# Performance work log

Hardware: AMD Instinct MI355X
Metric: run time of the kernel (lower is better)

The kernel has to match this reference:

```python
import jax, jax.numpy as jnp
import numpy as np

NUM_HEADS = 16
HEAD_DIM = 64
HIDDEN = NUM_HEADS * HEAD_DIM  # 1024
BATCH, SEQ = 4, 2048


def setup_inputs() -> dict:
    key = jax.random.key(0)
    k1, k2, k3, k4 = jax.random.split(key, 4)
    hidden_states = jax.random.normal(k1, (BATCH, SEQ, HIDDEN), dtype=jnp.float32)
    attention_mask = jnp.arange(SEQ)[None, :] < int(SEQ * 0.9)
    attention_mask = jnp.broadcast_to(attention_mask, (BATCH, SEQ))
    s_in = 1.0 / np.sqrt(HIDDEN)
    Wqkv = jax.random.normal(k2, (HIDDEN, 3 * HIDDEN), dtype=jnp.float32) * s_in
    Wout = jax.random.normal(k3, (HIDDEN, HIDDEN), dtype=jnp.float32) * s_in
    bout = jnp.zeros((HIDDEN,), dtype=jnp.float32)
    return {"hidden_states": hidden_states, "attention_mask": attention_mask,
            "Wqkv": Wqkv, "Wout": Wout, "bout": bout}


def reference(hidden_states, attention_mask, Wqkv, Wout, bout):
    B, S, H = hidden_states.shape
    qkv = hidden_states @ Wqkv  # [B,S,3*H]
    qkv = qkv.reshape(B, S, 3, NUM_HEADS, HEAD_DIM)
    qkv = jnp.transpose(qkv, (2, 0, 3, 1, 4))  # [3,B,nh,S,hd]
    q, k, v = qkv[0], qkv[1], qkv[2]
    scale = 1.0 / jnp.sqrt(jnp.float32(HEAD_DIM))
    attn = jnp.einsum('bhid,bhjd->bhij', q, k) * scale  # [B,nh,S,S]
    bias = jnp.where(attention_mask[:, None, None, :], 0.0,
                     jnp.finfo(jnp.float32).min)
    attn = attn + bias
    attn = jax.nn.softmax(attn, axis=-1)
    out = jnp.einsum('bhij,bhjd->bhid', attn, v)  # [B,nh,S,hd]
    out = jnp.transpose(out, (0, 2, 1, 3)).reshape(B, S, H)
    return out @ Wout + bout
```

## Files before the change

kernel.cpp:

```cpp
#include <hip/hip_runtime.h>


typedef short bh8 __attribute__((ext_vector_type(8)));
typedef short bh4 __attribute__((ext_vector_type(4)));
typedef float f32x4 __attribute__((ext_vector_type(4)));

#define B_ 4
#define S_ 2048
#define NH_ 16
#define HD_ 64
#define H_ 1024

__device__ float g_biasf[B_ * S_];
__device__ int g_tl[B_ * 33];

__device__ inline short f2bf(float f) {
    unsigned u = __builtin_bit_cast(unsigned, f);
    u = (u + 0x7fffu + ((u >> 16) & 1u)) >> 16;
    return (short)u;
}

__device__ inline unsigned pk2bf(float a, float b) {
#if __has_builtin(__builtin_amdgcn_cvt_pk_bf16_f32)
    auto r = __builtin_amdgcn_cvt_pk_bf16_f32(a, b);
    return __builtin_bit_cast(unsigned, r);
#else
    unsigned ua = __builtin_bit_cast(unsigned, a) + 0x8000u;
    unsigned ub = __builtin_bit_cast(unsigned, b) + 0x8000u;
    return __builtin_amdgcn_perm(ub, ua, 0x07060302);
#endif
}

__global__ void prep_all(const float* __restrict__ hidden, const float* __restrict__ Wqkv,
                         const float* __restrict__ Wout, const int* __restrict__ mask,
                         short* __restrict__ Xbf, short* __restrict__ WqkvT,
                         short* __restrict__ WoutT, float qs) {
    __shared__ float tile[32][33];
    int bi = blockIdx.x, tid = threadIdx.x;

    if (bi < 8192) {
        int i = (bi * 256 + tid) * 4;
        float4 v = *(const float4*)(hidden + i);
        union { short s[4]; unsigned long long u; } r;
        r.s[0] = f2bf(v.x); r.s[1] = f2bf(v.y); r.s[2] = f2bf(v.z); r.s[3] = f2bf(v.w);
        *(unsigned long long*)(Xbf + i) = r.u;
        return;
    }
    if (bi < 12288) {
        const float* in; short* out; int N, qcols, idx;
        if (bi < 11264) { in = Wqkv; out = WqkvT; N = 3 * H_; qcols = H_; idx = bi - 8192;
        } else          { in = Wout; out = WoutT; N = H_;    qcols = 0;  idx = bi - 11264; }
        int xt = (bi < 11264) ? 96 : 32;
        int n0 = (idx % xt) * 32, k0 = (idx / xt) * 32;
        int tx = tid & 31, ty = tid >> 5;
#pragma unroll
        for (int i = 0; i < 32; i += 8)
            tile[ty + i][tx] = in[(long)(k0 + ty + i) * N + n0 + tx];
        __syncthreads();
#pragma unroll
        for (int i = 0; i < 32; i += 8) {
            int n = n0 + ty + i;
            float v = tile[tx][ty + i];
            if (n < qcols) v *= qs;
            out[(long)n * H_ + k0 + tx] = f2bf(v);
        }
        return;
    }
    if (bi < 12320) {
        int i = (bi - 12288) * 256 + tid;
        g_biasf[i] = mask[i] ? 0.0f : -1e30f;
        return;
    }
    {
        int b = bi - 12320;
        if (tid < 64) {
            int t = tid, flag = 0;
            if (t < 32) {
                bool anyA = false, anyM = false;
                for (int i = 0; i < 64; ++i) {
                    int m = mask[b * S_ + t * 64 + i];
                    anyA |= (m != 0); anyM |= (m == 0);
                }
                flag = anyA ? (anyM ? 1 : 2) : 0;
            }
            unsigned long long act = __ballot(flag != 0);
            int pos = __popcll(act & ((1ull << t) - 1ull));
            if (flag) g_tl[b * 33 + 1 + pos] = t | (flag << 16);
            if (t == 0) g_tl[b * 33] = __popcll(act);
        }
    }
}

__global__ __launch_bounds__(256, 2) void gemm_bf16(
    const short* __restrict__ A, const short* __restrict__ Bt,
    int M, int N, int K, int mode,
    short* __restrict__ qk, short* __restrict__ vt,
    const float* __restrict__ bias, float* __restrict__ out) {
    __shared__ short smem[128 * 136];
    short* sA[2] = { smem, smem + 4096 };
    short* sB[2] = { smem + 8192, smem + 12288 };
    int tid = threadIdx.x;
    int lane = tid & 63, wid = tid >> 6;
    int quad = lane >> 4, l15 = lane & 15;
    int wy = wid >> 1, wx = wid & 1;
    int m0 = blockIdx.y * 128, n0 = blockIdx.x * 128;

    f32x4 acc[4][4] = {};
    const short* Ag = A + (long)m0 * K;
    const short* Bg = Bt + (long)n0 * K;

    for (int k0 = 0; k0 < K; k0 += 64) {
#pragma unroll
        for (int half = 0; half < 2; ++half) {
#pragma unroll
            for (int i = 0; i < 2; ++i) {
                int flat = i * 256 + tid;
                int r = flat >> 2, c = (flat & 3) << 3;
                __builtin_amdgcn_global_load_lds(
                    (const __attribute__((address_space(1))) void*)(Ag + (long)r * K + k0 + half * 32 + c),
                    (__attribute__((address_space(3))) void*)(sA[half] + i * 2048 + wid * 512),
                    16, 0, 0);
                __builtin_amdgcn_global_load_lds(
                    (const __attribute__((address_space(1))) void*)(Bg + (long)r * K + k0 + half * 32 + c),
                    (__attribute__((address_space(3))) void*)(sB[half] + i * 2048 + wid * 512),
                    16, 0, 0);
            }
        }
        __syncthreads();
#pragma unroll
        for (int half = 0; half < 2; ++half) {
            bh8 af[4], bfr[4];
#pragma unroll
            for (int mi = 0; mi < 4; ++mi)
                af[mi] = *(const bh8*)(sA[half] + (wy * 64 + mi * 16 + l15) * 32 + quad * 8);
#pragma unroll
            for (int ni = 0; ni < 4; ++ni)
                bfr[ni] = *(const bh8*)(sB[half] + (wx * 64 + ni * 16 + l15) * 32 + quad * 8);
#pragma unroll
            for (int mi = 0; mi < 4; ++mi)
#pragma unroll
                for (int ni = 0; ni < 4; ++ni)
                    acc[mi][ni] = __builtin_amdgcn_mfma_f32_16x16x32_bf16(af[mi], bfr[ni], acc[mi][ni], 0, 0, 0);
        }
        __syncthreads();
    }

    if (mode == 0) {
        bool isV = (n0 >= 2048);
#pragma unroll
        for (int mi = 0; mi < 4; ++mi)
#pragma unroll
            for (int ni = 0; ni < 4; ++ni) {
                int c = wx * 64 + ni * 16 + l15;
                int rb = wy * 64 + mi * 16 + quad * 4;
                if (isV) {
                    unsigned lo = pk2bf(acc[mi][ni][0], acc[mi][ni][1]);
                    unsigned hi = pk2bf(acc[mi][ni][2], acc[mi][ni][3]);
                    uint2 uu = {lo, hi};
                    *(bh4*)(smem + c * 136 + rb) = __builtin_bit_cast(bh4, uu);
                } else {
#pragma unroll
                    for (int reg = 0; reg < 4; ++reg)
                        smem[(rb + reg) * 136 + c] = f2bf(acc[mi][ni][reg]);
                }
            }
        __syncthreads();
        int b = m0 >> 11, sbase = m0 & 2047;
#pragma unroll
        for (int j = 0; j < 8; ++j) {
            int f = (j * 256 + tid) * 8;
            int i0 = f >> 7, i1 = f & 127;
            bh8 v = *(const bh8*)(smem + i0 * 136 + i1);
            if (isV) {
                int cc = n0 - 2048 + i0;
                int h = cc >> 6, d = cc & 63;
                *(bh8*)(vt + ((long)(b * NH_ + h) * HD_ + d) * S_ + sbase + i1) = v;
            } else {
                *(bh8*)(qk + (long)(m0 + i0) * 2048 + n0 + i1) = v;
            }
        }
    } else {
#pragma unroll
        for (int mi = 0; mi < 4; ++mi)
#pragma unroll
            for (int ni = 0; ni < 4; ++ni) {
                int gc = n0 + wx * 64 + ni * 16 + l15;
                float bv = bias[gc];
#pragma unroll
                for (int reg = 0; reg < 4; ++reg) {
                    int gr = m0 + wy * 64 + mi * 16 + quad * 4 + reg;
                    out[(long)gr * N + gc] = acc[mi][ni][reg] + bv;
                }
            }
    }
}

__global__ __launch_bounds__(256, 2) void attn_fwd(
    const short* __restrict__ QK, const short* __restrict__ Vtw,
    short* __restrict__ Aout) {
    __shared__ short lK[2][64 * 72];
    __shared__ short lV[2][64 * 72];
    int tid = threadIdx.x;
    int lane = tid & 63, w = tid >> 6;
    int quad = lane >> 4, l15 = lane & 15;
    int p = blockIdx.x;
    int b = p >> 4, h = p & 15;
    int qbase = blockIdx.y * 256 + w * 64;

    const short* Kb = QK + (long)b * S_ * 2048 + 1024 + h * HD_;
    const short* Vb = Vtw + (long)p * HD_ * S_;

    int r0 = tid >> 3, g = tid & 7, c = g << 3;
    int voff = (g >> 2) * 32 + (g & 1) * 16 + ((g >> 1) & 1) * 4;
    const short* Kp0 = Kb + (long)r0 * 2048 + c;
    const short* Kp1 = Kp0 + 32l * 2048;
    const short* Vp0 = Vb + (long)r0 * S_ + c;
    const short* Vp1 = Vp0 + 32l * S_;

    bh8 qf[4][2];
#pragma unroll
    for (int mi = 0; mi < 4; ++mi)
#pragma unroll
        for (int ks = 0; ks < 2; ++ks)
            qf[mi][ks] = *(const bh8*)(QK + (long)(b * S_ + qbase + mi * 16 + l15) * 2048
                                       + h * HD_ + ks * 32 + quad * 8);

    f32x4 o[4][4] = {};
    f32x4 ls[4] = {};
    const bh8 ones = {0x3F80, 0x3F80, 0x3F80, 0x3F80, 0x3F80, 0x3F80, 0x3F80, 0x3F80};

    int cnt = g_tl[b * 33];
    int e0 = g_tl[b * 33 + 1];
    int j0 = (e0 & 0xffff) << 6, flag = e0 >> 16;
    bh8 kp[2], vp[2];
    kp[0] = *(const bh8*)(Kp0 + (long)j0 * 2048);
    kp[1] = *(const bh8*)(Kp1 + (long)j0 * 2048);
    vp[0] = *(const bh8*)(Vp0 + j0);
    vp[1] = *(const bh8*)(Vp1 + j0);
    {
        *(bh8*)(lK[0] + r0 * 72 + c) = kp[0];
        *(bh8*)(lK[0] + (r0 + 32) * 72 + c) = kp[1];
        *(bh4*)(lV[0] + r0 * 72 + voff)            = __builtin_shufflevector(vp[0], vp[0], 0, 1, 2, 3);
        *(bh4*)(lV[0] + r0 * 72 + voff + 8)        = __builtin_shufflevector(vp[0], vp[0], 4, 5, 6, 7);
        *(bh4*)(lV[0] + (r0 + 32) * 72 + voff)     = __builtin_shufflevector(vp[1], vp[1], 0, 1, 2, 3);
        *(bh4*)(lV[0] + (r0 + 32) * 72 + voff + 8) = __builtin_shufflevector(vp[1], vp[1], 4, 5, 6, 7);
    }
    int cur = 0;

    for (int it = 0; it < cnt; ++it) {
        __syncthreads();
        bool more = (it + 1 < cnt);
        int nj0 = 0, nflag = 0;
        if (more) {
            int en = g_tl[b * 33 + 2 + it];
            nj0 = (en & 0xffff) << 6; nflag = en >> 16;
            kp[0] = *(const bh8*)(Kp0 + (long)nj0 * 2048);
            kp[1] = *(const bh8*)(Kp1 + (long)nj0 * 2048);
            vp[0] = *(const bh8*)(Vp0 + nj0);
            vp[1] = *(const bh8*)(Vp1 + nj0);
        }
        const short* ck = lK[cur];
        const short* cv = lV[cur];

        bh4 pf[4][4];
#pragma unroll
        for (int nj = 0; nj < 4; ++nj) {
            f32x4 scn[4] = {};
#pragma unroll
            for (int ks = 0; ks < 2; ++ks) {
                bh8 kf = *(const bh8*)(ck + (nj * 16 + l15) * 72 + ks * 32 + quad * 8);
#pragma unroll
                for (int mi = 0; mi < 4; ++mi)
                    scn[mi] = __builtin_amdgcn_mfma_f32_16x16x32_bf16(kf, qf[mi][ks], scn[mi], 0, 0, 0);
            }
            if (flag == 1) {
                f32x4 bb = *(const f32x4*)(g_biasf + b * S_ + j0 + nj * 16 + quad * 4);
#pragma unroll
                for (int mi = 0; mi < 4; ++mi) {
#pragma unroll
                    for (int r = 0; r < 4; ++r) scn[mi][r] += bb[r];
                }
            }
#pragma unroll
            for (int mi = 0; mi < 4; ++mi) {
                unsigned u0 = pk2bf(__builtin_amdgcn_exp2f(scn[mi][0]),
                                    __builtin_amdgcn_exp2f(scn[mi][1]));
                unsigned u1 = pk2bf(__builtin_amdgcn_exp2f(scn[mi][2]),
                                    __builtin_amdgcn_exp2f(scn[mi][3]));
                uint2 uu = {u0, u1};
                pf[nj][mi] = __builtin_bit_cast(bh4, uu);
            }
        }

#pragma unroll
        for (int pr = 0; pr < 2; ++pr) {
            int njA = 2 * pr, njB = 2 * pr + 1;
            bh8 a[4];
#pragma unroll
            for (int mi = 0; mi < 4; ++mi)
                a[mi] = __builtin_shufflevector(pf[njA][mi], pf[njB][mi], 0, 1, 2, 3, 4, 5, 6, 7);
            __builtin_amdgcn_s_setprio(1);
#pragma unroll
            for (int mi = 0; mi < 4; ++mi)
                ls[mi] = __builtin_amdgcn_mfma_f32_16x16x32_bf16(a[mi], ones, ls[mi], 0, 0, 0);
#pragma unroll
            for (int nd = 0; nd < 4; ++nd) {
                bh8 vf = *(const bh8*)(cv + (nd * 16 + l15) * 72 + pr * 32 + quad * 8);
#pragma unroll
                for (int mi = 0; mi < 4; ++mi)
                    o[mi][nd] = __builtin_amdgcn_mfma_f32_16x16x32_bf16(a[mi], vf, o[mi][nd], 0, 0, 0);
            }
            __builtin_amdgcn_s_setprio(0);
        }

        if (more) {
            short* lk = lK[cur ^ 1];
            short* lv = lV[cur ^ 1];
            *(bh8*)(lk + r0 * 72 + c) = kp[0];
            *(bh8*)(lk + (r0 + 32) * 72 + c) = kp[1];
            *(bh4*)(lv + r0 * 72 + voff)            = __builtin_shufflevector(vp[0], vp[0], 0, 1, 2, 3);
            *(bh4*)(lv + r0 * 72 + voff + 8)        = __builtin_shufflevector(vp[0], vp[0], 4, 5, 6, 7);
            *(bh4*)(lv + (r0 + 32) * 72 + voff)     = __builtin_shufflevector(vp[1], vp[1], 0, 1, 2, 3);
            *(bh4*)(lv + (r0 + 32) * 72 + voff + 8) = __builtin_shufflevector(vp[1], vp[1], 4, 5, 6, 7);
        }
        j0 = nj0; flag = nflag; cur ^= 1;
    }

#pragma unroll
    for (int mi = 0; mi < 4; ++mi)
#pragma unroll
        for (int reg = 0; reg < 4; ++reg) {
            float inv = __builtin_amdgcn_rcpf(ls[mi][reg]);
            int s = qbase + mi * 16 + quad * 4 + reg;
#pragma unroll
            for (int nd = 0; nd < 4; ++nd) {
                int col = h * HD_ + nd * 16 + l15;
                Aout[((long)b * S_ + s) * H_ + col] = f2bf(o[mi][nd][reg] * inv);
            }
        }
}

extern "C" void kernel_launch(void* const* d_in, const int* in_sizes, int n_in,
                              void* d_out, int out_size, void* d_ws, size_t ws_size,
                              hipStream_t stream) {
    const float* hidden = (const float*)d_in[0];
    const int* mask = (const int*)d_in[1];
    const float* Wqkv = (const float*)d_in[2];
    const float* Wout = (const float*)d_in[3];
    const float* bout = (const float*)d_in[4];
    float* out = (float*)d_out;

    char* ws = (char*)d_ws;
    const size_t XBF = 0;
    const size_t WQKVT = 16777216;
    const size_t WOUTT = WQKVT + 6291456;
    const size_t QKO = WOUTT + 2097152;
    const size_t VT = QKO + 33554432;

    short* Xbf = (short*)(ws + XBF);
    short* WqkvT = (short*)(ws + WQKVT);
    short* WoutT = (short*)(ws + WOUTT);
    short* QK = (short*)(ws + QKO);
    short* Vt = (short*)(ws + VT);
    short* Aout = Xbf;

    const float Cs = 0.18033688011112042f;

    prep_all<<<dim3(12324), dim3(256), 0, stream>>>(
        hidden, Wqkv, Wout, mask, Xbf, WqkvT, WoutT, Cs);

    gemm_bf16<<<dim3(24, 64), dim3(256), 0, stream>>>(
        Xbf, WqkvT, B_ * S_, 3 * H_, H_, 0, QK, Vt, nullptr, nullptr);

    attn_fwd<<<dim3(64, 8), dim3(256), 0, stream>>>(QK, Vt, Aout);

    gemm_bf16<<<dim3(8, 64), dim3(256), 0, stream>>>(
        Aout, WoutT, B_ * S_, H_, H_, 1, nullptr, nullptr, bout, out);
}
```

Baseline: 250.5 us.

## Double-buffer GEMM LDS tiles to overlap global loads with MFMA compute

Restructures the bf16 GEMM main loop into a two-stage pipeline. The next K-tile is prefetched into the alternate LDS buffer via global_load_lds while the current tile is consumed, with explicit vmcnt waits and raw barriers replacing __syncthreads. This targets global-load latency that was previously exposed each iteration. In exchange it doubles LDS use to 64KB per block, which may limit the occupancy the launch bounds request.

```diff
diff --git a/kernel.cpp b/kernel.cpp
--- a/kernel.cpp
+++ b/kernel.cpp
@@ -91,14 +91,32 @@
     }
 }
 
+__device__ inline void gemm_stage(const short* Ag, const short* Bg, int K, int k0,
+                                  short* sAB, int tid, int wid) {
+#pragma unroll
+    for (int half = 0; half < 2; ++half) {
+#pragma unroll
+        for (int i = 0; i < 2; ++i) {
+            int flat = i * 256 + tid;
+            int r = flat >> 2, c = (flat & 3) << 3;
+            __builtin_amdgcn_global_load_lds(
+                (const __attribute__((address_space(1))) void*)(Ag + (long)r * K + k0 + half * 32 + c),
+                (__attribute__((address_space(3))) void*)(sAB + half * 4096 + i * 2048 + wid * 512),
+                16, 0, 0);
+            __builtin_amdgcn_global_load_lds(
+                (const __attribute__((address_space(1))) void*)(Bg + (long)r * K + k0 + half * 32 + c),
+                (__attribute__((address_space(3))) void*)(sAB + 8192 + half * 4096 + i * 2048 + wid * 512),
+                16, 0, 0);
+        }
+    }
+}
+
 __global__ __launch_bounds__(256, 2) void gemm_bf16(
     const short* __restrict__ A, const short* __restrict__ Bt,
     int M, int N, int K, int mode,
     short* __restrict__ qk, short* __restrict__ vt,
     const float* __restrict__ bias, float* __restrict__ out) {
-    __shared__ short smem[128 * 136];
-    short* sA[2] = { smem, smem + 4096 };
-    short* sB[2] = { smem + 8192, smem + 12288 };
+    __shared__ short smem[32768];
     int tid = threadIdx.x;
     int lane = tid & 63, wid = tid >> 6;
     int quad = lane >> 4, l15 = lane & 15;
@@ -108,41 +126,36 @@
     f32x4 acc[4][4] = {};
     const short* Ag = A + (long)m0 * K;
     const short* Bg = Bt + (long)n0 * K;
-
-    for (int k0 = 0; k0 < K; k0 += 64) {
-#pragma unroll
-        for (int half = 0; half < 2; ++half) {
-#pragma unroll
-            for (int i = 0; i < 2; ++i) {
-                int flat = i * 256 + tid;
-                int r = flat >> 2, c = (flat & 3) << 3;
-                __builtin_amdgcn_global_load_lds(
-                    (const __attribute__((address_space(1))) void*)(Ag + (long)r * K + k0 + half * 32 + c),
-                    (__attribute__((address_space(3))) void*)(sA[half] + i * 2048 + wid * 512),
-                    16, 0, 0);
-                __builtin_amdgcn_global_load_lds(
-                    (const __attribute__((address_space(1))) void*)(Bg + (long)r * K + k0 + half * 32 + c),
-                    (__attribute__((address_space(3))) void*)(sB[half] + i * 2048 + wid * 512),
-                    16, 0, 0);
-            }
-        }
-        __syncthreads();
+    int NT = K >> 6;
+
+    gemm_stage(Ag, Bg, K, 0, smem, tid, wid);
+    for (int t = 0; t < NT; ++t) {
+        int curOff = (t & 1) << 14;
+        if (t + 1 < NT) {
+            gemm_stage(Ag, Bg, K, (t + 1) << 6, smem + (curOff ^ 16384), tid, wid);
+            asm volatile("s_waitcnt vmcnt(8)" ::: "memory");
+        } else {
+            asm volatile("s_waitcnt vmcnt(0)" ::: "memory");
+        }
+        __builtin_amdgcn_s_barrier();
+        const short* sA = smem + curOff;
+        const short* sB = smem + curOff + 8192;
 #pragma unroll
         for (int half = 0; half < 2; ++half) {
             bh8 af[4], bfr[4];
 #pragma unroll
             for (int mi = 0; mi < 4; ++mi)
-                af[mi] = *(const bh8*)(sA[half] + (wy * 64 + mi * 16 + l15) * 32 + quad * 8);
+                af[mi] = *(const bh8*)(sA + half * 4096 + (wy * 64 + mi * 16 + l15) * 32 + quad * 8);
 #pragma unroll
             for (int ni = 0; ni < 4; ++ni)
-                bfr[ni] = *(const bh8*)(sB[half] + (wx * 64 + ni * 16 + l15) * 32 + quad * 8);
+                bfr[ni] = *(const bh8*)(sB + half * 4096 + (wx * 64 + ni * 16 + l15) * 32 + quad * 8);
 #pragma unroll
             for (int mi = 0; mi < 4; ++mi)
 #pragma unroll
                 for (int ni = 0; ni < 4; ++ni)
                     acc[mi][ni] = __builtin_amdgcn_mfma_f32_16x16x32_bf16(af[mi], bfr[ni], acc[mi][ni], 0, 0, 0);
         }
-        __syncthreads();
+        __builtin_amdgcn_s_barrier();
     }
 
     if (mode == 0) {
```

New measurement: 253.4 us. No clear change (+1.2%).

## Specialize QKV GEMM with 256x256 tiles, direct-to-LDS loads and block swizzle

Applied to the files above, without the earlier changes.

Splits the generic GEMM into a dedicated QKV projection kernel and an output-projection kernel. The QKV kernel uses 512 threads, 256x256 tiles, double-buffered global_load_lds staging prefetched two K-steps ahead, a swizzled block order for L2 reuse, and raised wave priority around the MFMA bursts. The goal is more data reuse per tile and load latency hidden behind the MFMAs. The costs are 128KB of LDS per block, which may cap occupancy at one block per CU, and only 384 blocks, which could leave CUs unevenly loaded.

```diff
diff --git a/kernel.cpp b/kernel.cpp
--- a/kernel.cpp
+++ b/kernel.cpp
@@ -91,11 +91,133 @@
     }
 }
 
-__global__ __launch_bounds__(256, 2) void gemm_bf16(
+__device__ inline void stage256(const short* Ag, const short* Bg, int k0,
+                                short* dst, int tid, int wid) {
+#pragma unroll
+    for (int j = 0; j < 4; ++j) {
+        int row = (j & 1) * 128 + (tid >> 2);
+        int col = k0 + (j >> 1) * 32 + (tid & 3) * 8;
+        __builtin_amdgcn_global_load_lds(
+            (const __attribute__((address_space(1))) void*)(Ag + (long)row * 1024 + col),
+            (__attribute__((address_space(3))) void*)(dst + j * 4096 + wid * 512),
+            16, 0, 0);
+        __builtin_amdgcn_global_load_lds(
+            (const __attribute__((address_space(1))) void*)(Bg + (long)row * 1024 + col),
+            (__attribute__((address_space(3))) void*)(dst + 16384 + j * 4096 + wid * 512),
+            16, 0, 0);
+    }
+}
+
+__global__ __launch_bounds__(512, 2) void gemm_qkv(
     const short* __restrict__ A, const short* __restrict__ Bt,
-    int M, int N, int K, int mode,
-    short* __restrict__ qk, short* __restrict__ vt,
-    const float* __restrict__ bias, float* __restrict__ out) {
+    short* __restrict__ qk, short* __restrict__ vt) {
+    __shared__ short smem[65536];
+    const int NT = 16;
+    int tid = threadIdx.x;
+    int lane = tid & 63, wid = tid >> 6;
+    int quad = lane >> 4, l15 = lane & 15;
+    int wr = wid >> 2, wc = wid & 3;
+    int lin = blockIdx.y * 12 + blockIdx.x;
+    int swz = (lin & 7) * 48 + (lin >> 3);
+    int m0 = (swz / 12) * 256, n0 = (swz % 12) * 256;
+
+    const short* Ag = A + (long)m0 * 1024;
+    const short* Bg = Bt + (long)n0 * 1024;
+
+    f32x4 acc[8][4] = {};
+
+    stage256(Ag, Bg, 0, smem, tid, wid);
+    stage256(Ag, Bg, 64, smem + 32768, tid, wid);
+    asm volatile("s_waitcnt vmcnt(8)" ::: "memory");
+    __builtin_amdgcn_s_barrier();
+
+    for (int t = 0; t < NT; ++t) {
+        const short* sA = smem + (t & 1) * 32768;
+        const short* sB = sA + 16384;
+        bh8 a0[8], b0[4];
+#pragma unroll
+        for (int mi = 0; mi < 8; ++mi)
+            a0[mi] = *(const bh8*)(sA + (wr * 128 + mi * 16 + l15) * 32 + quad * 8);
+#pragma unroll
+        for (int ni = 0; ni < 4; ++ni)
+            b0[ni] = *(const bh8*)(sB + (wc * 64 + ni * 16 + l15) * 32 + quad * 8);
+        __builtin_amdgcn_s_setprio(1);
+#pragma unroll
+        for (int mi = 0; mi < 8; ++mi)
+#pragma unroll
+            for (int ni = 0; ni < 4; ++ni)
+                acc[mi][ni] = __builtin_amdgcn_mfma_f32_16x16x32_bf16(a0[mi], b0[ni], acc[mi][ni], 0, 0, 0);
+        __builtin_amdgcn_s_setprio(0);
+        bh8 a1[8], b1[4];
+#pragma unroll
+        for (int mi = 0; mi < 8; ++mi)
+            a1[mi] = *(const bh8*)(sA + 8192 + (wr * 128 + mi * 16 + l15) * 32 + quad * 8);
+#pragma unroll
+        for (int ni = 0; ni < 4; ++ni)
+            b1[ni] = *(const bh8*)(sB + 8192 + (wc * 64 + ni * 16 + l15) * 32 + quad * 8);
+        asm volatile("s_waitcnt lgkmcnt(0)" ::: "memory");
+        __builtin_amdgcn_sched_barrier(0);
+        __builtin_amdgcn_s_barrier();
+        if (t + 2 < NT)
+            stage256(Ag, Bg, (t + 2) << 6, smem + (t & 1) * 32768, tid, wid);
+        __builtin_amdgcn_s_setprio(1);
+#pragma unroll
+        for (int mi = 0; mi < 8; ++mi)
+#pragma unroll
+            for (int ni = 0; ni < 4; ++ni)
+                acc[mi][ni] = __builtin_amdgcn_mfma_f32_16x16x32_bf16(a1[mi], b1[ni], acc[mi][ni], 0, 0, 0);
+        __builtin_amdgcn_s_setprio(0);
+        if (t + 2 < NT)      { asm volatile("s_waitcnt vmcnt(8)" ::: "memory"); }
+        else if (t + 1 < NT) { asm volatile("s_waitcnt vmcnt(0)" ::: "memory"); }
+        __builtin_amdgcn_s_barrier();
+    }
+
+    __syncthreads();
+    bool isV = (n0 >= 2048);
+    if (!isV) {
+#pragma unroll
+        for (int mi = 0; mi < 8; ++mi)
+#pragma unroll
+            for (int ni = 0; ni < 4; ++ni) {
+                int r = wr * 128 + mi * 16 + quad * 4;
+                int c = wc * 64 + ni * 16 + l15;
+#pragma unroll
+                for (int reg = 0; reg < 4; ++reg)
+                    smem[(r + reg) * 256 + c] = f2bf(acc[mi][ni][reg]);
+            }
+    } else {
+#pragma unroll
+        for (int mi = 0; mi < 8; ++mi)
+#pragma unroll
+            for (int ni = 0; ni < 4; ++ni) {
+                int r = wr * 128 + mi * 16 + quad * 4;
+                int c = wc * 64 + ni * 16 + l15;
+                unsigned lo = pk2bf(acc[mi][ni][0], acc[mi][ni][1]);
+                unsigned hi = pk2bf(acc[mi][ni][2], acc[mi][ni][3]);
+                uint2 uu = {lo, hi};
+                *(bh4*)(smem + c * 256 + r) = __builtin_bit_cast(bh4, uu);
+            }
+    }
+    __syncthreads();
+    int bb = m0 >> 11, sbase = m0 & 2047;
+#pragma unroll
+    for (int j = 0; j < 16; ++j) {
+        int cj = j * 512 + tid;
+        int i0 = cj >> 5, i1 = (cj & 31) << 3;
+        bh8 v = *(const bh8*)(smem + i0 * 256 + i1);
+        if (isV) {
+            int cc = n0 - 2048 + i0;
+            int h = cc >> 6, d = cc & 63;
+            *(bh8*)(vt + ((long)(bb * NH_ + h) * HD_ + d) * S_ + sbase + i1) = v;
+        } else {
+            *(bh8*)(qk + (long)(m0 + i0) * 2048 + n0 + i1) = v;
+        }
+    }
+}
+
+__global__ __launch_bounds__(256, 2) void gemm_out(
+    const short* __restrict__ A, const short* __restrict__ Bt,
+    int N, int K, const float* __restrict__ bias, float* __restrict__ out) {
     __shared__ short smem[128 * 136];
     short* sA[2] = { smem, smem + 4096 };
     short* sB[2] = { smem + 8192, smem + 12288 };
@@ -145,54 +267,18 @@
         __syncthreads();
     }
 
-    if (mode == 0) {
-        bool isV = (n0 >= 2048);
-#pragma unroll
-        for (int mi = 0; mi < 4; ++mi)
-#pragma unroll
-            for (int ni = 0; ni < 4; ++ni) {
-                int c = wx * 64 + ni * 16 + l15;
-                int rb = wy * 64 + mi * 16 + quad * 4;
-                if (isV) {
-                    unsigned lo = pk2bf(acc[mi][ni][0], acc[mi][ni][1]);
-                    unsigned hi = pk2bf(acc[mi][ni][2], acc[mi][ni][3]);
-                    uint2 uu = {lo, hi};
-                    *(bh4*)(smem + c * 136 + rb) = __builtin_bit_cast(bh4, uu);
-                } else {
-#pragma unroll
-                    for (int reg = 0; reg < 4; ++reg)
-                        smem[(rb + reg) * 136 + c] = f2bf(acc[mi][ni][reg]);
-                }
-            }
-        __syncthreads();
-        int b = m0 >> 11, sbase = m0 & 2047;
-#pragma unroll
-        for (int j = 0; j < 8; ++j) {
-            int f = (j * 256 + tid) * 8;
-            int i0 = f >> 7, i1 = f & 127;
-            bh8 v = *(const bh8*)(smem + i0 * 136 + i1);
-            if (isV) {
-                int cc = n0 - 2048 + i0;
-                int h = cc >> 6, d = cc & 63;
-                *(bh8*)(vt + ((long)(b * NH_ + h) * HD_ + d) * S_ + sbase + i1) = v;
-            } else {
-                *(bh8*)(qk + (long)(m0 + i0) * 2048 + n0 + i1) = v;
-            }
-        }
-    } else {
-#pragma unroll
-        for (int mi = 0; mi < 4; ++mi)
-#pragma unroll
-            for (int ni = 0; ni < 4; ++ni) {
-                int gc = n0 + wx * 64 + ni * 16 + l15;
-                float bv = bias[gc];
-#pragma unroll
-                for (int reg = 0; reg < 4; ++reg) {
-                    int gr = m0 + wy * 64 + mi * 16 + quad * 4 + reg;
-                    out[(long)gr * N + gc] = acc[mi][ni][reg] + bv;
-                }
-            }
-    }
+#pragma unroll
+    for (int mi = 0; mi < 4; ++mi)
+#pragma unroll
+        for (int ni = 0; ni < 4; ++ni) {
+            int gc = n0 + wx * 64 + ni * 16 + l15;
+            float bv = bias[gc];
+#pragma unroll
+            for (int reg = 0; reg < 4; ++reg) {
+                int gr = m0 + wy * 64 + mi * 16 + quad * 4 + reg;
+                out[(long)gr * N + gc] = acc[mi][ni][reg] + bv;
+            }
+        }
 }
 
 __global__ __launch_bounds__(256, 2) void attn_fwd(
@@ -369,11 +455,10 @@
     prep_all<<<dim3(12324), dim3(256), 0, stream>>>(
         hidden, Wqkv, Wout, mask, Xbf, WqkvT, WoutT, Cs);
 
-    gemm_bf16<<<dim3(24, 64), dim3(256), 0, stream>>>(
-        Xbf, WqkvT, B_ * S_, 3 * H_, H_, 0, QK, Vt, nullptr, nullptr);
+    gemm_qkv<<<dim3(12, 32), dim3(512), 0, stream>>>(Xbf, WqkvT, QK, Vt);
 
     attn_fwd<<<dim3(64, 8), dim3(256), 0, stream>>>(QK, Vt, Aout);
 
-    gemm_bf16<<<dim3(8, 64), dim3(256), 0, stream>>>(
-        Aout, WoutT, B_ * S_, H_, H_, 1, nullptr, nullptr, bout, out);
-}
+    gemm_out<<<dim3(8, 64), dim3(256), 0, stream>>>(
+        Aout, WoutT, H_, H_, bout, out);
+}
```

Result: slower. 267.8 us (+6.9%).
